# Performance work log

Measured on AMD Instinct MI355X. Metric: run time of the kernel, lower is better.

The kernel has to match this reference:

```python
import jax, jax.numpy as jnp
import numpy as np

N_NODES = 100000
N_EDGES = 640000
D_IN = 128
D_OUT = 128

def setup_inputs() -> dict:
    key = jax.random.key(0)
    k1, k2, k3, k4, k5 = jax.random.split(key, 5)
    feat = jax.random.normal(k1, (N_NODES, D_IN), dtype=jnp.float32)
    src = jax.random.randint(k2, (N_EDGES,), 0, N_NODES, dtype=jnp.int32)
    dst = jax.random.randint(k3, (N_EDGES,), 0, N_NODES, dtype=jnp.int32)
    scale = 1.0 / np.sqrt(D_IN)
    W_self = jax.random.normal(k4, (D_IN, D_OUT), dtype=jnp.float32) * scale
    W_neigh = jax.random.normal(k5, (D_IN, D_OUT), dtype=jnp.float32) * scale
    b_self = jnp.zeros((D_OUT,), dtype=jnp.float32)
    b_neigh = jnp.zeros((D_OUT,), dtype=jnp.float32)
    return {"feat": feat, "src": src, "dst": dst,
            "W_self": W_self, "b_self": b_self,
            "W_neigh": W_neigh, "b_neigh": b_neigh}

def reference(feat, src, dst, W_self, b_self, W_neigh, b_neigh):
    # GraphSAGE 'mean' aggregator: copy_src + mean reduce over in-edges, then
    # rst = fc_self(h_self) + fc_neigh(h_neigh). feat_drop=0, no activation/norm.
    n = feat.shape[0]
    msg = feat[src]                                   # [E, D_in] gather
    neigh_sum = jax.ops.segment_sum(msg, dst, num_segments=n)      # [N, D_in]
    deg = jax.ops.segment_sum(jnp.ones_like(dst, dtype=feat.dtype), dst,
                              num_segments=n)          # [N]
    # mean with zero-in-degree nodes -> 0 (DGL semantics)
    h_neigh = neigh_sum / jnp.maximum(deg, 1.0)[:, None]
    rst = feat @ W_self + b_self + h_neigh @ W_neigh + b_neigh      # [N, D_out]
    return rst
```

## Files before the change

### kernel.cpp

```cpp
#include <hip/hip_runtime.h>


constexpr int N_NODES = 100000;
constexpr int N_EDGES = 640000;
constexpr int D = 128;

constexpr int SCAN_ELEMS_PER_BLOCK = 1024;
constexpr int SCAN_NBLOCKS = (N_NODES + SCAN_ELEMS_PER_BLOCK - 1) / SCAN_ELEMS_PER_BLOCK;

typedef __attribute__((ext_vector_type(8))) short bf16x8;
typedef __attribute__((ext_vector_type(4))) float f32x4;
typedef __attribute__((ext_vector_type(2))) float f32x2;

__device__ __forceinline__ unsigned short f2bf(float f) {
    unsigned int u = __float_as_uint(f);
    unsigned int r = u + 0x7FFFu + ((u >> 16) & 1u);
    return (unsigned short)(r >> 16);
}

__global__ void deg_wprep_kernel(const int* __restrict__ dst, int* __restrict__ deg,
                                 const float* __restrict__ Ws, const float* __restrict__ Wn,
                                 unsigned short* __restrict__ wp) {
    int e = blockIdx.x * blockDim.x + threadIdx.x;
    if (e < N_EDGES) atomicAdd(&deg[dst[e]], 1);
    if (e < 2 * D * D) {
        int i = e;
        int r  = i & 7;
        int c  = (i >> 3) & 127;
        int h  = (i >> 10) & 3;
        int ks = (i >> 12) & 3;
        int m  = i >> 14;
        const float* W = m ? Wn : Ws;
        int k = ks * 32 + h * 8 + r;
        wp[i] = f2bf(W[k * D + c]);
    }
}


__global__ __launch_bounds__(256) void partial_kernel(const int* __restrict__ deg,
                                                      int* __restrict__ bsum) {
    __shared__ int wsum[4];
    const int tid = threadIdx.x;
    const int base = (blockIdx.x * 256 + tid) * 4;
    int s = 0;
    #pragma unroll
    for (int j = 0; j < 4; j++) {
        int idx = base + j;
        if (idx < N_NODES) s += deg[idx];
    }
    for (int off = 32; off > 0; off >>= 1) s += __shfl_down(s, off, 64);
    if ((tid & 63) == 0) wsum[tid >> 6] = s;
    __syncthreads();
    if (tid == 0) bsum[blockIdx.x] = wsum[0] + wsum[1] + wsum[2] + wsum[3];
}

__global__ __launch_bounds__(128) void scanb_kernel(const int* __restrict__ bsum,
                                                    int* __restrict__ boff,
                                                    int* __restrict__ rowptr) {
    __shared__ int s[128];
    const int tid = threadIdx.x;
    int v = (tid < SCAN_NBLOCKS) ? bsum[tid] : 0;
    s[tid] = v;
    __syncthreads();
    for (int off = 1; off < 128; off <<= 1) {
        int u = (tid >= off) ? s[tid - off] : 0;
        __syncthreads();
        s[tid] += u;
        __syncthreads();
    }
    if (tid < SCAN_NBLOCKS) boff[tid] = s[tid] - v;
    if (tid == 0) rowptr[N_NODES] = N_EDGES;
}

__global__ __launch_bounds__(256) void final_kernel(const int* __restrict__ deg,
                                                    const int* __restrict__ boff,
                                                    int* __restrict__ rowptr,
                                                    int* __restrict__ cursor) {
    __shared__ int wsum[4];
    const int tid = threadIdx.x;
    const int lane = tid & 63;
    const int wave = tid >> 6;
    const int base = (blockIdx.x * 256 + tid) * 4;

    int local[4];
    int tsum = 0;
    #pragma unroll
    for (int j = 0; j < 4; j++) {
        int idx = base + j;
        local[j] = (idx < N_NODES) ? deg[idx] : 0;
        tsum += local[j];
    }
    int incl = tsum;
    for (int off = 1; off < 64; off <<= 1) {
        int u = __shfl_up(incl, off, 64);
        if (lane >= off) incl += u;
    }
    if (lane == 63) wsum[wave] = incl;
    __syncthreads();
    int woff = 0;
    for (int w = 0; w < 4; w++) woff += (w < wave) ? wsum[w] : 0;

    int run = boff[blockIdx.x] + woff + (incl - tsum);
    #pragma unroll
    for (int j = 0; j < 4; j++) {
        int idx = base + j;
        if (idx < N_NODES) {
            rowptr[idx] = run;
            cursor[idx] = run;
            run += local[j];
        }
    }
}

__global__ void fill_kernel(const int* __restrict__ src, const int* __restrict__ dst,
                            int* __restrict__ cursor, int* __restrict__ csr_src) {
    int e = blockIdx.x * blockDim.x + threadIdx.x;
    if (e < N_EDGES) {
        int pos = atomicAdd(&cursor[dst[e]], 1);
        csr_src[pos] = src[e];
    }
}

__global__ __launch_bounds__(256) void mmfused_kernel(
    const float* __restrict__ feat, const unsigned short* __restrict__ wp,
    const float* __restrict__ b_self, const float* __restrict__ b_neigh,
    float* __restrict__ out, unsigned short* __restrict__ t)
{
    __shared__ unsigned short lw[2 * 4 * 4 * 128 * 8];

    const int tid = threadIdx.x;
    {
        const uint4* s = (const uint4*)wp;
        uint4* d = (uint4*)lw;
        #pragma unroll
        for (int i = 0; i < 16; i++) d[tid + i * 256] = s[tid + i * 256];
    }
    __syncthreads();

    const int wave = tid >> 6, lane = tid & 63;
    const int h = lane >> 4, c = lane & 15;
    const int row_base = blockIdx.x * 128 + wave * 32;

    bf16x8 a[2][4];
    #pragma unroll
    for (int ti = 0; ti < 2; ti++) {
        int row = row_base + ti * 16 + c;
        int rowc = min(row, N_NODES - 1);
        const float4* fr = (const float4*)(feat + (size_t)rowc * D);
        #pragma unroll
        for (int ks = 0; ks < 4; ks++) {
            float4 u = fr[ks * 8 + h * 2];
            float4 v = fr[ks * 8 + h * 2 + 1];
            bf16x8 f;
            f[0] = (short)f2bf(u.x); f[1] = (short)f2bf(u.y);
            f[2] = (short)f2bf(u.z); f[3] = (short)f2bf(u.w);
            f[4] = (short)f2bf(v.x); f[5] = (short)f2bf(v.y);
            f[6] = (short)f2bf(v.z); f[7] = (short)f2bf(v.w);
            a[ti][ks] = f;
        }
    }

    #pragma unroll
    for (int m = 0; m < 2; m++) {
        for (int ct = 0; ct < 8; ct++) {
            bf16x8 b[4];
            #pragma unroll
            for (int ks = 0; ks < 4; ks++)
                b[ks] = ((const bf16x8*)lw)[((m * 4 + ks) * 4 + h) * 128 + ct * 16 + c];

            f32x4 acc[2];
            #pragma unroll
            for (int ti = 0; ti < 2; ti++) acc[ti] = f32x4{0.f, 0.f, 0.f, 0.f};
            #pragma unroll
            for (int ks = 0; ks < 4; ks++)
                #pragma unroll
                for (int ti = 0; ti < 2; ti++)
                    acc[ti] = __builtin_amdgcn_mfma_f32_16x16x32_bf16(a[ti][ks], b[ks], acc[ti], 0, 0, 0);

            const int col = ct * 16 + c;
            if (m == 0) {
                const float bias = b_self[col] + b_neigh[col];
                #pragma unroll
                for (int ti = 0; ti < 2; ti++) {
                    if (row_base + ti * 16 < N_NODES) {
                        #pragma unroll
                        for (int q = 0; q < 4; q++) {
                            int row = row_base + ti * 16 + h * 4 + q;
                            out[(size_t)row * D + col] = acc[ti][q] + bias;
                        }
                    }
                }
            } else {
                #pragma unroll
                for (int ti = 0; ti < 2; ti++) {
                    if (row_base + ti * 16 < N_NODES) {
                        #pragma unroll
                        for (int q = 0; q < 4; q++) {
                            int row = row_base + ti * 16 + h * 4 + q;
                            t[(size_t)row * D + col] = f2bf(acc[ti][q]);
                        }
                    }
                }
            }
        }
    }
}

__global__ __launch_bounds__(256) void gather_kernel(
    const unsigned short* __restrict__ t, const int* __restrict__ csr_src,
    const int* __restrict__ rowptr, float* __restrict__ out)
{
    const int lane = threadIdx.x & 63;
    const int n = (blockIdx.x * blockDim.x + threadIdx.x) >> 6;
    if (n >= N_NODES) return;

    const int e0 = rowptr[n];
    const int e1 = rowptr[n + 1];

    f32x2* orow = (f32x2*)(out + (size_t)n * D) + lane;
    f32x2 o = __builtin_nontemporal_load(orow);

    float ax = 0.f, ay = 0.f;
    for (int base = e0; base < e1; base += 8) {
        int sidx[8];
        #pragma unroll
        for (int j = 0; j < 8; j++) {
            int ee = base + j;
            ee = (ee < e1) ? ee : (e1 - 1);
            sidx[j] = csr_src[ee];
        }
        unsigned int v[8];
        #pragma unroll
        for (int j = 0; j < 8; j++)
            v[j] = ((const unsigned int*)(t + (size_t)sidx[j] * D))[lane];
        #pragma unroll
        for (int j = 0; j < 8; j++) {
            const float w = (base + j < e1) ? 1.0f : 0.0f;
            ax = fmaf(w, __uint_as_float(v[j] << 16), ax);
            ay = fmaf(w, __uint_as_float(v[j] & 0xFFFF0000u), ay);
        }
    }
    const float sc = 1.0f / (float)max(e1 - e0, 1);
    o.x += ax * sc;
    o.y += ay * sc;
    __builtin_nontemporal_store(o, orow);
}

extern "C" void kernel_launch(void* const* d_in, const int* in_sizes, int n_in,
                              void* d_out, int out_size, void* d_ws, size_t ws_size,
                              hipStream_t stream) {
    const float* feat    = (const float*)d_in[0];
    const int*   src     = (const int*)d_in[1];
    const int*   dst     = (const int*)d_in[2];
    const float* W_self  = (const float*)d_in[3];
    const float* b_self  = (const float*)d_in[4];
    const float* W_neigh = (const float*)d_in[5];
    const float* b_neigh = (const float*)d_in[6];
    float* out = (float*)d_out;

    unsigned short* t  = (unsigned short*)d_ws;
    unsigned short* wp = t + (size_t)N_NODES * D;
    int*   deg     = (int*)(wp + 2 * D * D);
    int*   rowptr  = deg + N_NODES;
    int*   cursor  = rowptr + (N_NODES + 1);
    int*   csr_src = cursor + N_NODES;
    int*   bsum    = csr_src + N_EDGES;
    int*   boff    = bsum + SCAN_NBLOCKS;

    (void)hipMemsetAsync(deg, 0, N_NODES * sizeof(int), stream);

    deg_wprep_kernel<<<(N_EDGES + 255) / 256, 256, 0, stream>>>(dst, deg, W_self, W_neigh, wp);

    partial_kernel<<<SCAN_NBLOCKS, 256, 0, stream>>>(deg, bsum);
    scanb_kernel<<<1, 128, 0, stream>>>(bsum, boff, rowptr);
    final_kernel<<<SCAN_NBLOCKS, 256, 0, stream>>>(deg, boff, rowptr, cursor);

    fill_kernel<<<(N_EDGES + 255) / 256, 256, 0, stream>>>(src, dst, cursor, csr_src);

    mmfused_kernel<<<(N_NODES + 127) / 128, 256, 0, stream>>>(feat, wp, b_self, b_neigh, out, t);

    gather_kernel<<<25000, 256, 0, stream>>>(t, csr_src, rowptr, out);
}
```

Before: 147.9 us.

## Aggregate bf16 features before projecting, fusing both matmuls into one pass

Reorders the computation from project-then-aggregate to aggregate-then-project. The prepass kernel now also converts feat to a bf16 copy. The gather kernel averages bf16 neighbour features into a bf16 h_neigh buffer, and a single MFMA kernel then computes feat@W_self + h_neigh@W_neigh with the bias. This drops the read-modify-write of the fp32 output in the gather pass and the separate bf16 projected-neighbour write. In exchange it adds a full feature conversion pass and an extra bf16 rounding of the mean aggregate.

Result: faster. 138.2 us (-6.6%).

```diff
diff --git a/kernel.cpp b/kernel.cpp
--- a/kernel.cpp
+++ b/kernel.cpp
@@ -10,7 +10,6 @@
 
 typedef __attribute__((ext_vector_type(8))) short bf16x8;
 typedef __attribute__((ext_vector_type(4))) float f32x4;
-typedef __attribute__((ext_vector_type(2))) float f32x2;
 
 __device__ __forceinline__ unsigned short f2bf(float f) {
     unsigned int u = __float_as_uint(f);
@@ -18,13 +17,14 @@
     return (unsigned short)(r >> 16);
 }
 
-__global__ void deg_wprep_kernel(const int* __restrict__ dst, int* __restrict__ deg,
-                                 const float* __restrict__ Ws, const float* __restrict__ Wn,
-                                 unsigned short* __restrict__ wp) {
-    int e = blockIdx.x * blockDim.x + threadIdx.x;
-    if (e < N_EDGES) atomicAdd(&deg[dst[e]], 1);
-    if (e < 2 * D * D) {
-        int i = e;
+__global__ void prepass_kernel(const int* __restrict__ dst, int* __restrict__ deg,
+                               const float* __restrict__ Ws, const float* __restrict__ Wn,
+                               unsigned short* __restrict__ wp,
+                               const float* __restrict__ feat, unsigned short* __restrict__ fb) {
+    const int gid = blockIdx.x * blockDim.x + threadIdx.x;
+    if (gid < N_EDGES) atomicAdd(&deg[dst[gid]], 1);
+    if (gid < 2 * D * D) {
+        int i = gid;
         int r  = i & 7;
         int c  = (i >> 3) & 127;
         int h  = (i >> 10) & 3;
@@ -34,6 +34,13 @@
         int k = ks * 32 + h * 8 + r;
         wp[i] = f2bf(W[k * D + c]);
     }
+    const int total4 = N_NODES * D / 4;
+    for (int i = gid; i < total4; i += N_EDGES) {
+        float4 v = ((const float4*)feat)[i];
+        ushort4 o;
+        o.x = f2bf(v.x); o.y = f2bf(v.y); o.z = f2bf(v.z); o.w = f2bf(v.w);
+        ((ushort4*)fb)[i] = o;
+    }
 }
 
 
@@ -121,10 +128,48 @@
     }
 }
 
+__global__ __launch_bounds__(256) void gather_kernel(
+    const unsigned short* __restrict__ fb, const int* __restrict__ csr_src,
+    const int* __restrict__ rowptr, unsigned short* __restrict__ hn)
+{
+    const int lane = threadIdx.x & 63;
+    const int n = (blockIdx.x * blockDim.x + threadIdx.x) >> 6;
+    if (n >= N_NODES) return;
+
+    const int e0 = rowptr[n];
+    const int e1 = rowptr[n + 1];
+
+    float ax = 0.f, ay = 0.f;
+    for (int base = e0; base < e1; base += 8) {
+        int sidx[8];
+        #pragma unroll
+        for (int j = 0; j < 8; j++) {
+            int ee = base + j;
+            ee = (ee < e1) ? ee : (e1 - 1);
+            sidx[j] = csr_src[ee];
+        }
+        unsigned int v[8];
+        #pragma unroll
+        for (int j = 0; j < 8; j++)
+            v[j] = ((const unsigned int*)(fb + (size_t)sidx[j] * D))[lane];
+        #pragma unroll
+        for (int j = 0; j < 8; j++) {
+            const float w = (base + j < e1) ? 1.0f : 0.0f;
+            ax = fmaf(w, __uint_as_float(v[j] << 16), ax);
+            ay = fmaf(w, __uint_as_float(v[j] & 0xFFFF0000u), ay);
+        }
+    }
+    const float sc = 1.0f / (float)max(e1 - e0, 1);
+    const unsigned int packed =
+        ((unsigned int)f2bf(ay * sc) << 16) | (unsigned int)f2bf(ax * sc);
+    ((unsigned int*)(hn + (size_t)n * D))[lane] = packed;
+}
+
 __global__ __launch_bounds__(256) void mmfused_kernel(
-    const float* __restrict__ feat, const unsigned short* __restrict__ wp,
+    const unsigned short* __restrict__ fb, const unsigned short* __restrict__ hn,
+    const unsigned short* __restrict__ wp,
     const float* __restrict__ b_self, const float* __restrict__ b_neigh,
-    float* __restrict__ out, unsigned short* __restrict__ t)
+    float* __restrict__ out)
 {
     __shared__ unsigned short lw[2 * 4 * 4 * 128 * 8];
 
@@ -141,109 +186,51 @@
     const int h = lane >> 4, c = lane & 15;
     const int row_base = blockIdx.x * 128 + wave * 32;
 
-    bf16x8 a[2][4];
+    bf16x8 a[2][2][4];
     #pragma unroll
     for (int ti = 0; ti < 2; ti++) {
         int row = row_base + ti * 16 + c;
         int rowc = min(row, N_NODES - 1);
-        const float4* fr = (const float4*)(feat + (size_t)rowc * D);
+        const bf16x8* f0 = (const bf16x8*)(fb + (size_t)rowc * D);
+        const bf16x8* f1 = (const bf16x8*)(hn + (size_t)rowc * D);
         #pragma unroll
         for (int ks = 0; ks < 4; ks++) {
-            float4 u = fr[ks * 8 + h * 2];
-            float4 v = fr[ks * 8 + h * 2 + 1];
-            bf16x8 f;
-            f[0] = (short)f2bf(u.x); f[1] = (short)f2bf(u.y);
-            f[2] = (short)f2bf(u.z); f[3] = (short)f2bf(u.w);
-            f[4] = (short)f2bf(v.x); f[5] = (short)f2bf(v.y);
-            f[6] = (short)f2bf(v.z); f[7] = (short)f2bf(v.w);
-            a[ti][ks] = f;
-        }
-    }
-
-    #pragma unroll
-    for (int m = 0; m < 2; m++) {
-        for (int ct = 0; ct < 8; ct++) {
+            a[0][ti][ks] = f0[ks * 4 + h];
+            a[1][ti][ks] = f1[ks * 4 + h];
+        }
+    }
+
+    for (int ct = 0; ct < 8; ct++) {
+        f32x4 acc[2];
+        #pragma unroll
+        for (int ti = 0; ti < 2; ti++) acc[ti] = f32x4{0.f, 0.f, 0.f, 0.f};
+
+        #pragma unroll
+        for (int m = 0; m < 2; m++) {
             bf16x8 b[4];
             #pragma unroll
             for (int ks = 0; ks < 4; ks++)
                 b[ks] = ((const bf16x8*)lw)[((m * 4 + ks) * 4 + h) * 128 + ct * 16 + c];
-
-            f32x4 acc[2];
-            #pragma unroll
-            for (int ti = 0; ti < 2; ti++) acc[ti] = f32x4{0.f, 0.f, 0.f, 0.f};
             #pragma unroll
             for (int ks = 0; ks < 4; ks++)
                 #pragma unroll
                 for (int ti = 0; ti < 2; ti++)
-                    acc[ti] = __builtin_amdgcn_mfma_f32_16x16x32_bf16(a[ti][ks], b[ks], acc[ti], 0, 0, 0);
-
-            const int col = ct * 16 + c;
-            if (m == 0) {
-                const float bias = b_self[col] + b_neigh[col];
+                    acc[ti] = __builtin_amdgcn_mfma_f32_16x16x32_bf16(a[m][ti][ks], b[ks], acc[ti], 0, 0, 0);
+        }
+
+        const int col = ct * 16 + c;
+        const float bias = b_self[col] + b_neigh[col];
+        #pragma unroll
+        for (int ti = 0; ti < 2; ti++) {
+            if (row_base + ti * 16 < N_NODES) {
                 #pragma unroll
-                for (int ti = 0; ti < 2; ti++) {
-                    if (row_base + ti * 16 < N_NODES) {
-                        #pragma unroll
-                        for (int q = 0; q < 4; q++) {
-                            int row = row_base + ti * 16 + h * 4 + q;
-                            out[(size_t)row * D + col] = acc[ti][q] + bias;
-                        }
-                    }
-                }
-            } else {
-                #pragma unroll
-                for (int ti = 0; ti < 2; ti++) {
-                    if (row_base + ti * 16 < N_NODES) {
-                        #pragma unroll
-                        for (int q = 0; q < 4; q++) {
-                            int row = row_base + ti * 16 + h * 4 + q;
-                            t[(size_t)row * D + col] = f2bf(acc[ti][q]);
-                        }
-                    }
+                for (int q = 0; q < 4; q++) {
+                    int row = row_base + ti * 16 + h * 4 + q;
+                    out[(size_t)row * D + col] = acc[ti][q] + bias;
                 }
             }
         }
     }
-}
-
-__global__ __launch_bounds__(256) void gather_kernel(
-    const unsigned short* __restrict__ t, const int* __restrict__ csr_src,
-    const int* __restrict__ rowptr, float* __restrict__ out)
-{
-    const int lane = threadIdx.x & 63;
-    const int n = (blockIdx.x * blockDim.x + threadIdx.x) >> 6;
-    if (n >= N_NODES) return;
-
-    const int e0 = rowptr[n];
-    const int e1 = rowptr[n + 1];
-
-    f32x2* orow = (f32x2*)(out + (size_t)n * D) + lane;
-    f32x2 o = __builtin_nontemporal_load(orow);
-
-    float ax = 0.f, ay = 0.f;
-    for (int base = e0; base < e1; base += 8) {
-        int sidx[8];
-        #pragma unroll
-        for (int j = 0; j < 8; j++) {
-            int ee = base + j;
-            ee = (ee < e1) ? ee : (e1 - 1);
-            sidx[j] = csr_src[ee];
-        }
-        unsigned int v[8];
-        #pragma unroll
-        for (int j = 0; j < 8; j++)
-            v[j] = ((const unsigned int*)(t + (size_t)sidx[j] * D))[lane];
-        #pragma unroll
-        for (int j = 0; j < 8; j++) {
-            const float w = (base + j < e1) ? 1.0f : 0.0f;
-            ax = fmaf(w, __uint_as_float(v[j] << 16), ax);
-            ay = fmaf(w, __uint_as_float(v[j] & 0xFFFF0000u), ay);
-        }
-    }
-    const float sc = 1.0f / (float)max(e1 - e0, 1);
-    o.x += ax * sc;
-    o.y += ay * sc;
-    __builtin_nontemporal_store(o, orow);
 }
 
 extern "C" void kernel_launch(void* const* d_in, const int* in_sizes, int n_in,
@@ -258,8 +245,9 @@
     const float* b_neigh = (const float*)d_in[6];
     float* out = (float*)d_out;
 
-    unsigned short* t  = (unsigned short*)d_ws;
-    unsigned short* wp = t + (size_t)N_NODES * D;
+    unsigned short* fb = (unsigned short*)d_ws;
+    unsigned short* hn = fb + (size_t)N_NODES * D;
+    unsigned short* wp = hn + (size_t)N_NODES * D;
     int*   deg     = (int*)(wp + 2 * D * D);
     int*   rowptr  = deg + N_NODES;
     int*   cursor  = rowptr + (N_NODES + 1);
@@ -269,7 +257,8 @@
 
     (void)hipMemsetAsync(deg, 0, N_NODES * sizeof(int), stream);
 
-    deg_wprep_kernel<<<(N_EDGES + 255) / 256, 256, 0, stream>>>(dst, deg, W_self, W_neigh, wp);
+    prepass_kernel<<<(N_EDGES + 255) / 256, 256, 0, stream>>>(dst, deg, W_self, W_neigh,
+                                                              wp, feat, fb);
 
     partial_kernel<<<SCAN_NBLOCKS, 256, 0, stream>>>(deg, bsum);
     scanb_kernel<<<1, 128, 0, stream>>>(bsum, boff, rowptr);
@@ -277,7 +266,7 @@
 
     fill_kernel<<<(N_EDGES + 255) / 256, 256, 0, stream>>>(src, dst, cursor, csr_src);
 
-    mmfused_kernel<<<(N_NODES + 127) / 128, 256, 0, stream>>>(feat, wp, b_self, b_neigh, out, t);
-
-    gather_kernel<<<25000, 256, 0, stream>>>(t, csr_src, rowptr, out);
-}
+    gather_kernel<<<25000, 256, 0, stream>>>(fb, csr_src, rowptr, hn);
+
+    mmfused_kernel<<<(N_NODES + 127) / 128, 256, 0, stream>>>(fb, hn, wp, b_self, b_neigh, out);
+}
```
